# Performance work log

Measured on AMD Instinct MI355X. Metric: run time of the kernel, lower is better.

The kernel has to match this reference:

```python
import jax, jax.numpy as jnp
import numpy as np

B, T, C, H, D = 4, 2048, 1024, 16, 64
EPS = 1e-5

def setup_inputs() -> dict:
    key = jax.random.key(0)
    ks = jax.random.split(key, 8)
    s = lambda fan_in: 1.0 / np.sqrt(fan_in)
    return {
        'x': jax.random.normal(ks[0], (B, T, C), jnp.float32),
        'wq': jax.random.normal(ks[1], (H, C, D), jnp.float32) * s(C),
        'wk': jax.random.normal(ks[2], (H, C, D), jnp.float32) * s(C),
        'wv': jax.random.normal(ks[3], (H, C, D), jnp.float32) * s(C),
        'w_proj': jax.random.normal(ks[4], (C, C), jnp.float32) * s(C),
        'b_proj': jnp.zeros((C,), jnp.float32),
        'w1': jax.random.normal(ks[5], (C, 4 * C), jnp.float32) * s(C),
        'b1': jnp.zeros((4 * C,), jnp.float32),
        'w2': jax.random.normal(ks[6], (4 * C, C), jnp.float32) * s(4 * C),
        'b2': jnp.zeros((C,), jnp.float32),
        'g1': jnp.ones((C,), jnp.float32),
        'be1': jnp.zeros((C,), jnp.float32),
        'g2': jnp.ones((C,), jnp.float32),
        'be2': jnp.zeros((C,), jnp.float32),
    }

def layer_norm(x, g, b):
    mu = jnp.mean(x, axis=-1, keepdims=True)
    var = jnp.mean(jnp.square(x - mu), axis=-1, keepdims=True)
    return (x - mu) * jax.lax.rsqrt(var + EPS) * g + b

def reference(x, wq, wk, wv, w_proj, b_proj, w1, b1, w2, b2, g1, be1, g2, be2):
    # --- attention (pre-LN) ---
    xn = layer_norm(x, g1, be1)
    q = jnp.einsum('btc,hcd->bhtd', xn, wq)
    k = jnp.einsum('btc,hcd->bhtd', xn, wk)
    v = jnp.einsum('btc,hcd->bhtd', xn, wv)
    # NOTE: original scales by full embedding dim C (not head size)
    scores = jnp.einsum('bhtd,bhsd->bhts', q, k) * (C ** -0.5)
    causal = jnp.tril(jnp.ones((T, T), bool))
    scores = jnp.where(causal, scores, -jnp.inf)
    wei = jax.nn.softmax(scores, axis=-1)
    attn = jnp.einsum('bhts,bhsd->bhtd', wei, v)
    attn = attn.transpose(0, 2, 1, 3).reshape(B, T, C)  # concat heads
    x = x + attn @ w_proj + b_proj
    # --- FFN (pre-LN) ---
    xn2 = layer_norm(x, g2, be2)
    h = jax.nn.relu(xn2 @ w1 + b1)
    x = x + h @ w2 + b2
    return x
```

## Files before the change

kernel.cpp:

```cpp
#include <hip/hip_runtime.h>
#include <hip/hip_bf16.h>

#define B_ 4
#define T_ 2048
#define C_ 1024
#define H_ 16
#define D_ 64
#define M_ (B_*T_)

typedef unsigned short ushort;
typedef __attribute__((ext_vector_type(8))) short short8;
typedef __attribute__((ext_vector_type(8))) unsigned short ushort8;
typedef __attribute__((ext_vector_type(4))) float floatx4;
typedef __attribute__((ext_vector_type(4))) unsigned int uintx4;

static __device__ __forceinline__ float bf2f(ushort u) {
    unsigned int x = ((unsigned int)u) << 16;
    return __builtin_bit_cast(float, x);
}
static __device__ __forceinline__ ushort f2bf(float f) {
    unsigned int x = __builtin_bit_cast(unsigned int, f);
    unsigned int r = (x + 0x7fffu + ((x >> 16) & 1u)) >> 16;
    return (ushort)r;
}

typedef const __attribute__((address_space(1))) unsigned int gu32;
typedef __attribute__((address_space(3))) unsigned int lu32;
static __device__ __forceinline__ void glds16(const void* g, void* l) {
    __builtin_amdgcn_global_load_lds((gu32*)g, (lu32*)l, 16, 0, 0);
}

__global__ __launch_bounds__(256) void ln_kernel(
    const float* __restrict__ x, const float* __restrict__ g,
    const float* __restrict__ be, ushort* __restrict__ out)
{
    int row = blockIdx.x;
    int tid = threadIdx.x;
    const float* xr = x + (size_t)row * C_;
    float v[4];
    float s = 0.f, s2 = 0.f;
#pragma unroll
    for (int i = 0; i < 4; i++) {
        float t = xr[tid + i * 256];
        v[i] = t; s += t; s2 += t * t;
    }
#pragma unroll
    for (int off = 32; off; off >>= 1) {
        s  += __shfl_down(s, off);
        s2 += __shfl_down(s2, off);
    }
    __shared__ float rs[4], rs2[4];
    __shared__ float smu, srstd;
    int w = tid >> 6;
    if ((tid & 63) == 0) { rs[w] = s; rs2[w] = s2; }
    __syncthreads();
    if (tid == 0) {
        float ts  = rs[0] + rs[1] + rs[2] + rs[3];
        float ts2 = rs2[0] + rs2[1] + rs2[2] + rs2[3];
        float mu  = ts * (1.f / C_);
        float var = ts2 * (1.f / C_) - mu * mu;
        smu = mu; srstd = rsqrtf(var + 1e-5f);
    }
    __syncthreads();
    float mu = smu, r = srstd;
#pragma unroll
    for (int i = 0; i < 4; i++) {
        int c = tid + i * 256;
        out[(size_t)row * C_ + c] = f2bf((v[i] - mu) * r * g[c] + be[c]);
    }
}

static __device__ __forceinline__ void do_transpose(
    const float* __restrict__ in, ushort* __restrict__ out,
    int R, int Cn, int bx, int by)
{
    __shared__ float tile[32][33];
    int tx = threadIdx.x;
    int ty = threadIdx.y;
    int c0 = bx * 32, r0 = by * 32;
#pragma unroll
    for (int i = 0; i < 32; i += 8) {
        tile[ty + i][tx] = in[(size_t)(r0 + ty + i) * Cn + c0 + tx];
    }
    __syncthreads();
#pragma unroll
    for (int i = 0; i < 32; i += 8) {
        int oc = c0 + ty + i;
        int orr = r0 + tx;
        out[(size_t)oc * R + orr] = f2bf(tile[tx][ty + i]);
    }
}

__global__ __launch_bounds__(256) void wt_fused_kernel(
    const float* __restrict__ wq, const float* __restrict__ wk, const float* __restrict__ wv,
    const float* __restrict__ w_proj, const float* __restrict__ w1, const float* __restrict__ w2,
    ushort* __restrict__ WqkvT, ushort* __restrict__ WprojT,
    ushort* __restrict__ W1T, ushort* __restrict__ W2T)
{
    int id = blockIdx.x;
    if (id < 3072) {
        int which = id >> 10;
        int lid = id & 1023;
        int bz = lid >> 6;
        int rem = lid & 63;
        int by = rem >> 1, bx = rem & 1;
        const float* in = (which == 0 ? wq : which == 1 ? wk : wv) + (size_t)bz * C_ * D_;
        ushort* out = WqkvT + (size_t)which * C_ * C_ + (size_t)bz * D_ * C_;
        do_transpose(in, out, C_, D_, bx, by);
    } else if (id < 4096) {
        int lid = id - 3072;
        do_transpose(w_proj, WprojT, C_, C_, lid & 31, lid >> 5);
    } else if (id < 8192) {
        int lid = id - 4096;
        do_transpose(w1, W1T, C_, 4 * C_, lid & 127, lid >> 7);
    } else {
        int lid = id - 8192;
        do_transpose(w2, W2T, 4 * C_, C_, lid & 31, lid >> 5);
    }
}

__global__ __launch_bounds__(256) void vtrans_kernel(
    const ushort* __restrict__ qkv, ushort* __restrict__ VtG)
{
    int bh = blockIdx.y;
    int b = bh >> 4, h = bh & 15;
    int j0 = blockIdx.x * 64;
    int tid = threadIdx.x;
    __shared__ unsigned int X[64 * 33];
    const ushort* Vg = qkv + (size_t)(b * T_) * 3072 + 2048 + h * 64;
#pragma unroll
    for (int it = 0; it < 2; it++) {
        int j = (tid >> 3) + it * 32;
        int dp = (tid & 7) * 4;
        uintx4 val = *(const uintx4*)(Vg + (size_t)(j0 + j) * 3072 + dp * 2);
#pragma unroll
        for (int k = 0; k < 4; k++) X[j * 33 + dp + k] = val[k];
    }
    __syncthreads();
    int dp = tid >> 3, jc = tid & 7;
    unsigned int v[8];
#pragma unroll
    for (int jj = 0; jj < 8; jj++) v[jj] = X[(jc * 8 + jj) * 33 + dp];
    ushort8 lo, hi;
#pragma unroll
    for (int jj = 0; jj < 8; jj++) {
        lo[jj] = (ushort)(v[jj] & 0xffffu);
        hi[jj] = (ushort)(v[jj] >> 16);
    }
    size_t r0 = ((size_t)(h * 256 + 4 * (2 * dp) + b)) * T_ + j0 + jc * 8;
    size_t r1 = ((size_t)(h * 256 + 4 * (2 * dp + 1) + b)) * T_ + j0 + jc * 8;
    *(ushort8*)&VtG[r0] = lo;
    *(ushort8*)&VtG[r1] = hi;
}

template<bool OUTBF16, bool BIAS, bool RELU, bool RESID, bool DBUF>
__global__ __launch_bounds__(256, 2) void gemm_kernel(
    const ushort* __restrict__ A,
    const ushort* __restrict__ Bt,
    const float* __restrict__ bias,
    const float* __restrict__ resid,
    void* __restrict__ Cout,
    int Ndim, int K, int Nt)
{
    constexpr int NB = DBUF ? 2 : 1;
    __shared__ ushort As[NB][128 * 64];
    __shared__ ushort Bs[NB][128 * 64];
    int bid = blockIdx.x;
    int xcd = bid & 7;
    int loc = bid >> 3;
    int m0 = (xcd * 8 + (loc & 7)) * 128;
    int n0 = (loc >> 3) * 128;

    int tid = threadIdx.x;
    int wave = tid >> 6, lane = tid & 63;
    int quad = lane >> 4, l16 = lane & 15;
    int wm = (wave >> 1) * 64, wn = (wave & 1) * 64;
    floatx4 acc[4][4] = {};

    int lrow = lane >> 3;
    int lchunk = (lane & 7) ^ (lrow & 7);
    const ushort* Ab = A  + (size_t)m0 * K + lchunk * 8;
    const ushort* Bb = Bt + (size_t)n0 * K + lchunk * 8;

    int nK = K >> 6;
    if (DBUF) {
#pragma unroll
        for (int it = 0; it < 4; it++) {
            int rb = wave * 32 + it * 8;
            int r  = rb + lrow;
            glds16(Ab + (size_t)r * K, &As[0][rb * 64]);
            glds16(Bb + (size_t)r * K, &Bs[0][rb * 64]);
        }
    }

    for (int ki = 0; ki < nK; ki++) {
        int buf = DBUF ? (ki & 1) : 0;
        __syncthreads();
        if (DBUF) {
            if (ki + 1 < nK) {
                int kn = (ki + 1) * 64;
#pragma unroll
                for (int it = 0; it < 4; it++) {
                    int rb = wave * 32 + it * 8;
                    int r  = rb + lrow;
                    glds16(Ab + (size_t)r * K + kn, &As[buf ^ 1][rb * 64]);
                    glds16(Bb + (size_t)r * K + kn, &Bs[buf ^ 1][rb * 64]);
                }
            }
        } else {
            int kn = ki * 64;
#pragma unroll
            for (int it = 0; it < 4; it++) {
                int rb = wave * 32 + it * 8;
                int r  = rb + lrow;
                glds16(Ab + (size_t)r * K + kn, &As[0][rb * 64]);
                glds16(Bb + (size_t)r * K + kn, &Bs[0][rb * 64]);
            }
            __syncthreads();
        }
#pragma unroll
        for (int kk = 0; kk < 2; kk++) {
            short8 af[4], bfv[4];
            int c = kk * 4 + quad;
            int sw = (c ^ (l16 & 7)) * 8;
#pragma unroll
            for (int mi = 0; mi < 4; mi++)
                af[mi] = *(const short8*)&As[buf][(wm + mi * 16 + l16) * 64 + sw];
#pragma unroll
            for (int ni = 0; ni < 4; ni++)
                bfv[ni] = *(const short8*)&Bs[buf][(wn + ni * 16 + l16) * 64 + sw];
#pragma unroll
            for (int mi = 0; mi < 4; mi++)
#pragma unroll
                for (int ni = 0; ni < 4; ni++)
                    acc[mi][ni] = __builtin_amdgcn_mfma_f32_16x16x32_bf16(af[mi], bfv[ni], acc[mi][ni], 0, 0, 0);
        }
    }

    int r4 = quad * 4;
#pragma unroll
    for (int mi = 0; mi < 4; mi++) {
#pragma unroll
        for (int ni = 0; ni < 4; ni++) {
#pragma unroll
            for (int r = 0; r < 4; r++) {
                int gm = m0 + wm + mi * 16 + r4 + r;
                int gn = n0 + wn + ni * 16 + l16;
                float v = acc[mi][ni][r];
                if (BIAS)  v += bias[gn];
                if (RESID) v += resid[(size_t)gm * Ndim + gn];
                if (RELU)  v = fmaxf(v, 0.f);
                if (OUTBF16) ((ushort*)Cout)[(size_t)gm * Ndim + gn] = f2bf(v);
                else         ((float*)Cout)[(size_t)gm * Ndim + gn] = v;
            }
        }
    }
}

__global__ __launch_bounds__(256, 2) void attn_kernel(
    const ushort* __restrict__ qkv,
    const ushort* __restrict__ VtG,
    ushort* __restrict__ attnb)
{
    const int LD = 3072;
    int bid = blockIdx.x;
    int bh = (bid & 7) * 8 + ((bid >> 3) & 7);
    int qt = 15 - (bid >> 6);
    int b = bh >> 4, h = bh & 15;
    int t0 = qt * 128;
    int tid = threadIdx.x;
    int wave = tid >> 6, lane = tid & 63;
    int quad = lane >> 4, l16 = lane & 15;

    __shared__ ushort Ks[2][64 * 64];
    __shared__ ushort Vt[2][64 * 64];
    __shared__ ushort Ps[4][32 * 72];

    const ushort* Qg = qkv + (size_t)(b * T_) * LD + h * 64;
    const ushort* Kg = Qg + 1024;
    const ushort* VtB = VtG + (size_t)(h * 256 + b) * T_;

    int qrow_base = t0 + wave * 32;
    int lrow = lane >> 3;
    int lchunk = (lane & 7) ^ (lrow & 7);

    short8 qa[2][2];
#pragma unroll
    for (int mt = 0; mt < 2; mt++) {
        const ushort* qp = Qg + (size_t)(qrow_base + mt * 16 + l16) * LD + quad * 8;
        ushort8 q0 = *(const ushort8*)qp;
        ushort8 q1 = *(const ushort8*)(qp + 32);
        ushort8 a0, a1;
#pragma unroll
        for (int d = 0; d < 8; d++) {
            a0[d] = f2bf(bf2f(q0[d]) * 0.03125f);
            a1[d] = f2bf(bf2f(q1[d]) * 0.03125f);
        }
        qa[mt][0] = __builtin_bit_cast(short8, a0);
        qa[mt][1] = __builtin_bit_cast(short8, a1);
    }

    float l_part[2][4];
    floatx4 o_acc[2][4];
#pragma unroll
    for (int mt = 0; mt < 2; mt++)
#pragma unroll
        for (int r = 0; r < 4; r++) {
            l_part[mt][r] = 0.f;
            o_acc[mt][r] = floatx4{0.f, 0.f, 0.f, 0.f};
        }

    int nIter = t0 / 64 + 2;

#pragma unroll
    for (int it = 0; it < 2; it++) {
        int rb = (wave * 2 + it) * 8;
        int r = rb + lrow;
        glds16(Kg  + (size_t)r * LD + lchunk * 8, &Ks[0][rb * 64]);
        glds16(VtB + (size_t)r * (4 * T_) + lchunk * 8, &Vt[0][rb * 64]);
    }

    for (int ii = 0; ii < nIter; ii++) {
        int s0 = ii * 64;
        int buf = ii & 1;
        __syncthreads();
        if (ii + 1 < nIter) {
            int sn = s0 + 64;
#pragma unroll
            for (int it = 0; it < 2; it++) {
                int rb = (wave * 2 + it) * 8;
                int r = rb + lrow;
                glds16(Kg  + (size_t)(sn + r) * LD + lchunk * 8, &Ks[buf ^ 1][rb * 64]);
                glds16(VtB + (size_t)r * (4 * T_) + sn + lchunk * 8, &Vt[buf ^ 1][rb * 64]);
            }
        }

        if (s0 <= qrow_base + 31) {
#pragma unroll
            for (int mt = 0; mt < 2; mt++) {
                floatx4 s_acc[4];
#pragma unroll
                for (int nt = 0; nt < 4; nt++) {
                    int krow = nt * 16 + l16;
                    const short8* kb0 = (const short8*)&Ks[buf][krow * 64 + ((quad       ^ (l16 & 7)) * 8)];
                    const short8* kb1 = (const short8*)&Ks[buf][krow * 64 + (((4 + quad) ^ (l16 & 7)) * 8)];
                    floatx4 z = {0.f, 0.f, 0.f, 0.f};
                    z = __builtin_amdgcn_mfma_f32_16x16x32_bf16(qa[mt][0], *kb0, z, 0, 0, 0);
                    s_acc[nt] = __builtin_amdgcn_mfma_f32_16x16x32_bf16(qa[mt][1], *kb1, z, 0, 0, 0);
                }
                int base_mt = qrow_base + mt * 16;
                if (s0 + 63 > base_mt) {
#pragma unroll
                    for (int nt = 0; nt < 4; nt++)
#pragma unroll
                        for (int r = 0; r < 4; r++) {
                            int gi = base_mt + quad * 4 + r;
                            int gj = s0 + nt * 16 + l16;
                            if (gj > gi) s_acc[nt][r] = -INFINITY;
                        }
                }
#pragma unroll
                for (int nt = 0; nt < 4; nt++)
#pragma unroll
                    for (int r = 0; r < 4; r++) {
                        float e = __expf(s_acc[nt][r]);
                        s_acc[nt][r] = e;
                        l_part[mt][r] += e;
                        Ps[wave][(mt * 16 + quad * 4 + r) * 72 + nt * 16 + l16] = f2bf(e);
                    }
            }
            asm volatile("s_waitcnt lgkmcnt(0)" ::: "memory");
            short8 pa[2][2];
#pragma unroll
            for (int mt = 0; mt < 2; mt++) {
                pa[mt][0] = *(const short8*)&Ps[wave][(mt * 16 + l16) * 72 + quad * 8];
                pa[mt][1] = *(const short8*)&Ps[wave][(mt * 16 + l16) * 72 + quad * 8 + 32];
            }
#pragma unroll
            for (int dt = 0; dt < 4; dt++) {
                int vrow = dt * 16 + l16;
                const short8* vb0 = (const short8*)&Vt[buf][vrow * 64 + ((quad       ^ (l16 & 7)) * 8)];
                const short8* vb1 = (const short8*)&Vt[buf][vrow * 64 + (((4 + quad) ^ (l16 & 7)) * 8)];
#pragma unroll
                for (int mt = 0; mt < 2; mt++) {
                    o_acc[mt][dt] = __builtin_amdgcn_mfma_f32_16x16x32_bf16(pa[mt][0], *vb0, o_acc[mt][dt], 0, 0, 0);
                    o_acc[mt][dt] = __builtin_amdgcn_mfma_f32_16x16x32_bf16(pa[mt][1], *vb1, o_acc[mt][dt], 0, 0, 0);
                }
            }
        }
    }

#pragma unroll
    for (int mt = 0; mt < 2; mt++)
#pragma unroll
        for (int r = 0; r < 4; r++) {
            float ls = l_part[mt][r];
            ls += __shfl_xor(ls, 1);
            ls += __shfl_xor(ls, 2);
            ls += __shfl_xor(ls, 4);
            ls += __shfl_xor(ls, 8);
            float inv = 1.f / ls;
            int gi = qrow_base + mt * 16 + quad * 4 + r;
            ushort* op = attnb + (size_t)(b * T_ + gi) * 1024 + h * 64;
#pragma unroll
            for (int dt = 0; dt < 4; dt++)
                op[dt * 16 + l16] = f2bf(o_acc[mt][dt][r] * inv);
        }
}

extern "C" void kernel_launch(void* const* d_in, const int* in_sizes, int n_in,
                              void* d_out, int out_size, void* d_ws, size_t ws_size,
                              hipStream_t stream) {
    (void)in_sizes; (void)n_in; (void)out_size; (void)ws_size;
    const float* x      = (const float*)d_in[0];
    const float* wq     = (const float*)d_in[1];
    const float* wk     = (const float*)d_in[2];
    const float* wv     = (const float*)d_in[3];
    const float* w_proj = (const float*)d_in[4];
    const float* b_proj = (const float*)d_in[5];
    const float* w1     = (const float*)d_in[6];
    const float* b1     = (const float*)d_in[7];
    const float* w2     = (const float*)d_in[8];
    const float* b2     = (const float*)d_in[9];
    const float* g1     = (const float*)d_in[10];
    const float* be1    = (const float*)d_in[11];
    const float* g2     = (const float*)d_in[12];
    const float* be2    = (const float*)d_in[13];
    float* out = (float*)d_out;

    char* ws = (char*)d_ws;
    const size_t MB = 1024ull * 1024ull;
    ushort* xn     = (ushort*)(ws + 0);
    ushort* qkv    = (ushort*)(ws + 16 * MB);
    ushort* attnb  = (ushort*)(ws + 64 * MB);
    ushort* hbuf   = (ushort*)(ws + 16 * MB);
    float*  x1     = (float*) (ws + 80 * MB);
    ushort* VtG    = (ushort*)(ws + 80 * MB);
    ushort* WqkvT  = (ushort*)(ws + 112 * MB);
    ushort* WprojT = (ushort*)(ws + 118 * MB);
    ushort* W1T    = (ushort*)(ws + 120 * MB);
    ushort* W2T    = (ushort*)(ws + 128 * MB);
    ushort* xn2 = xn;

    ln_kernel<<<M_, 256, 0, stream>>>(x, g1, be1, xn);
    wt_fused_kernel<<<12288, dim3(32, 8), 0, stream>>>(
        wq, wk, wv, w_proj, w1, w2, WqkvT, WprojT, W1T, W2T);
    gemm_kernel<true, false, false, false, false><<<64 * 24, 256, 0, stream>>>(
        xn, WqkvT, nullptr, nullptr, qkv, 3072, C_, 24);
    vtrans_kernel<<<dim3(T_ / 64, B_ * H_), 256, 0, stream>>>(qkv, VtG);
    attn_kernel<<<1024, 256, 0, stream>>>(qkv, VtG, attnb);
    gemm_kernel<false, true, false, true, true><<<64 * 8, 256, 0, stream>>>(
        attnb, WprojT, b_proj, x, x1, C_, C_, 8);
    ln_kernel<<<M_, 256, 0, stream>>>(x1, g2, be2, xn2);
    gemm_kernel<true, true, true, false, false><<<64 * 32, 256, 0, stream>>>(
        xn2, W1T, b1, nullptr, hbuf, 4 * C_, C_, 32);
    gemm_kernel<false, true, false, true, true><<<64 * 8, 256, 0, stream>>>(
        hbuf, W2T, b2, x1, out, C_, 4 * C_, 8);
}
```

Baseline: 465.8 us.

## Fuse LN1 into weight prep kernel and double attention query tile to 256 rows

The first LayerNorm and the weight transpose/convert are merged into one launch, with blocks dispatched by ID range, which removes a kernel launch. The attention kernel now processes 256 query rows per block (64 per wave) instead of 128, so each K/V tile loaded into LDS is reused across twice as many queries. The grid is halved to 512 blocks and launch bounds ask for 3 blocks per CU. The risks are higher register pressure from the doubled accumulators and coarser causal load balance with fewer, larger blocks.

```diff
diff --git a/kernel.cpp b/kernel.cpp
--- a/kernel.cpp
+++ b/kernel.cpp
@@ -30,12 +30,10 @@
     __builtin_amdgcn_global_load_lds((gu32*)g, (lu32*)l, 16, 0, 0);
 }
 
-__global__ __launch_bounds__(256) void ln_kernel(
+static __device__ __forceinline__ void ln_body(
     const float* __restrict__ x, const float* __restrict__ g,
-    const float* __restrict__ be, ushort* __restrict__ out)
-{
-    int row = blockIdx.x;
-    int tid = threadIdx.x;
+    const float* __restrict__ be, ushort* __restrict__ out, int row, int tid)
+{
     const float* xr = x + (size_t)row * C_;
     float v[4];
     float s = 0.f, s2 = 0.f;
@@ -70,13 +68,20 @@
     }
 }
 
+__global__ __launch_bounds__(256) void ln_kernel(
+    const float* __restrict__ x, const float* __restrict__ g,
+    const float* __restrict__ be, ushort* __restrict__ out)
+{
+    ln_body(x, g, be, out, blockIdx.x, threadIdx.x);
+}
+
 static __device__ __forceinline__ void do_transpose(
     const float* __restrict__ in, ushort* __restrict__ out,
-    int R, int Cn, int bx, int by)
+    int R, int Cn, int bx, int by, int tid)
 {
     __shared__ float tile[32][33];
-    int tx = threadIdx.x;
-    int ty = threadIdx.y;
+    int tx = tid & 31;
+    int ty = tid >> 5;
     int c0 = bx * 32, r0 = by * 32;
 #pragma unroll
     for (int i = 0; i < 32; i += 8) {
@@ -91,31 +96,37 @@
     }
 }
 
-__global__ __launch_bounds__(256) void wt_fused_kernel(
+__global__ __launch_bounds__(256) void prep_fused_kernel(
+    const float* __restrict__ x, const float* __restrict__ g1, const float* __restrict__ be1,
+    ushort* __restrict__ xn,
     const float* __restrict__ wq, const float* __restrict__ wk, const float* __restrict__ wv,
     const float* __restrict__ w_proj, const float* __restrict__ w1, const float* __restrict__ w2,
     ushort* __restrict__ WqkvT, ushort* __restrict__ WprojT,
     ushort* __restrict__ W1T, ushort* __restrict__ W2T)
 {
     int id = blockIdx.x;
-    if (id < 3072) {
-        int which = id >> 10;
-        int lid = id & 1023;
-        int bz = lid >> 6;
-        int rem = lid & 63;
+    int tid = threadIdx.x;
+    if (id < 8192) {
+        ln_body(x, g1, be1, xn, id, tid);
+    } else if (id < 11264) {
+        int lid = id - 8192;
+        int which = lid >> 10;
+        int l2 = lid & 1023;
+        int bz = l2 >> 6;
+        int rem = l2 & 63;
         int by = rem >> 1, bx = rem & 1;
         const float* in = (which == 0 ? wq : which == 1 ? wk : wv) + (size_t)bz * C_ * D_;
         ushort* out = WqkvT + (size_t)which * C_ * C_ + (size_t)bz * D_ * C_;
-        do_transpose(in, out, C_, D_, bx, by);
-    } else if (id < 4096) {
-        int lid = id - 3072;
-        do_transpose(w_proj, WprojT, C_, C_, lid & 31, lid >> 5);
-    } else if (id < 8192) {
-        int lid = id - 4096;
-        do_transpose(w1, W1T, C_, 4 * C_, lid & 127, lid >> 7);
+        do_transpose(in, out, C_, D_, bx, by, tid);
+    } else if (id < 12288) {
+        int lid = id - 11264;
+        do_transpose(w_proj, WprojT, C_, C_, lid & 31, lid >> 5, tid);
+    } else if (id < 16384) {
+        int lid = id - 12288;
+        do_transpose(w1, W1T, C_, 4 * C_, lid & 127, lid >> 7, tid);
     } else {
-        int lid = id - 8192;
-        do_transpose(w2, W2T, 4 * C_, C_, lid & 31, lid >> 5);
+        int lid = id - 16384;
+        do_transpose(w2, W2T, 4 * C_, C_, lid & 31, lid >> 5, tid);
     }
 }
 
@@ -257,7 +268,7 @@
     }
 }
 
-__global__ __launch_bounds__(256, 2) void attn_kernel(
+__global__ __launch_bounds__(256, 3) void attn_kernel(
     const ushort* __restrict__ qkv,
     const ushort* __restrict__ VtG,
     ushort* __restrict__ attnb)
@@ -265,9 +276,9 @@
     const int LD = 3072;
     int bid = blockIdx.x;
     int bh = (bid & 7) * 8 + ((bid >> 3) & 7);
-    int qt = 15 - (bid >> 6);
+    int qt = 7 - (bid >> 6);
     int b = bh >> 4, h = bh & 15;
-    int t0 = qt * 128;
+    int t0 = qt * 256;
     int tid = threadIdx.x;
     int wave = tid >> 6, lane = tid & 63;
     int quad = lane >> 4, l16 = lane & 15;
@@ -280,13 +291,13 @@
     const ushort* Kg = Qg + 1024;
     const ushort* VtB = VtG + (size_t)(h * 256 + b) * T_;
 
-    int qrow_base = t0 + wave * 32;
+    int qrow_base = t0 + wave * 64;
     int lrow = lane >> 3;
     int lchunk = (lane & 7) ^ (lrow & 7);
 
-    short8 qa[2][2];
-#pragma unroll
-    for (int mt = 0; mt < 2; mt++) {
+    short8 qa[4][2];
+#pragma unroll
+    for (int mt = 0; mt < 4; mt++) {
         const ushort* qp = Qg + (size_t)(qrow_base + mt * 16 + l16) * LD + quad * 8;
         ushort8 q0 = *(const ushort8*)qp;
         ushort8 q1 = *(const ushort8*)(qp + 32);
@@ -300,17 +311,17 @@
         qa[mt][1] = __builtin_bit_cast(short8, a1);
     }
 
-    float l_part[2][4];
-    floatx4 o_acc[2][4];
-#pragma unroll
-    for (int mt = 0; mt < 2; mt++)
+    float l_part[4][4];
+    floatx4 o_acc[4][4];
+#pragma unroll
+    for (int mt = 0; mt < 4; mt++)
 #pragma unroll
         for (int r = 0; r < 4; r++) {
             l_part[mt][r] = 0.f;
             o_acc[mt][r] = floatx4{0.f, 0.f, 0.f, 0.f};
         }
 
-    int nIter = t0 / 64 + 2;
+    int nIter = t0 / 64 + 4;
 
 #pragma unroll
     for (int it = 0; it < 2; it++) {
@@ -335,63 +346,67 @@
             }
         }
 
-        if (s0 <= qrow_base + 31) {
-#pragma unroll
-            for (int mt = 0; mt < 2; mt++) {
-                floatx4 s_acc[4];
-#pragma unroll
-                for (int nt = 0; nt < 4; nt++) {
-                    int krow = nt * 16 + l16;
-                    const short8* kb0 = (const short8*)&Ks[buf][krow * 64 + ((quad       ^ (l16 & 7)) * 8)];
-                    const short8* kb1 = (const short8*)&Ks[buf][krow * 64 + (((4 + quad) ^ (l16 & 7)) * 8)];
-                    floatx4 z = {0.f, 0.f, 0.f, 0.f};
-                    z = __builtin_amdgcn_mfma_f32_16x16x32_bf16(qa[mt][0], *kb0, z, 0, 0, 0);
-                    s_acc[nt] = __builtin_amdgcn_mfma_f32_16x16x32_bf16(qa[mt][1], *kb1, z, 0, 0, 0);
-                }
-                int base_mt = qrow_base + mt * 16;
-                if (s0 + 63 > base_mt) {
+        if (s0 <= qrow_base + 63) {
+#pragma unroll
+            for (int h2 = 0; h2 < 2; h2++) {
+#pragma unroll
+                for (int mt2 = 0; mt2 < 2; mt2++) {
+                    int mt = h2 * 2 + mt2;
+                    floatx4 s_acc[4];
+#pragma unroll
+                    for (int nt = 0; nt < 4; nt++) {
+                        int krow = nt * 16 + l16;
+                        const short8* kb0 = (const short8*)&Ks[buf][krow * 64 + ((quad       ^ (l16 & 7)) * 8)];
+                        const short8* kb1 = (const short8*)&Ks[buf][krow * 64 + (((4 + quad) ^ (l16 & 7)) * 8)];
+                        floatx4 z = {0.f, 0.f, 0.f, 0.f};
+                        z = __builtin_amdgcn_mfma_f32_16x16x32_bf16(qa[mt][0], *kb0, z, 0, 0, 0);
+                        s_acc[nt] = __builtin_amdgcn_mfma_f32_16x16x32_bf16(qa[mt][1], *kb1, z, 0, 0, 0);
+                    }
+                    int base_mt = qrow_base + mt * 16;
+                    if (s0 + 63 > base_mt) {
+#pragma unroll
+                        for (int nt = 0; nt < 4; nt++)
+#pragma unroll
+                            for (int r = 0; r < 4; r++) {
+                                int gi = base_mt + quad * 4 + r;
+                                int gj = s0 + nt * 16 + l16;
+                                if (gj > gi) s_acc[nt][r] = -INFINITY;
+                            }
+                    }
 #pragma unroll
                     for (int nt = 0; nt < 4; nt++)
 #pragma unroll
                         for (int r = 0; r < 4; r++) {
-                            int gi = base_mt + quad * 4 + r;
-                            int gj = s0 + nt * 16 + l16;
-                            if (gj > gi) s_acc[nt][r] = -INFINITY;
+                            float e = __expf(s_acc[nt][r]);
+                            l_part[mt][r] += e;
+                            Ps[wave][(mt2 * 16 + quad * 4 + r) * 72 + nt * 16 + l16] = f2bf(e);
                         }
                 }
-#pragma unroll
-                for (int nt = 0; nt < 4; nt++)
-#pragma unroll
-                    for (int r = 0; r < 4; r++) {
-                        float e = __expf(s_acc[nt][r]);
-                        s_acc[nt][r] = e;
-                        l_part[mt][r] += e;
-                        Ps[wave][(mt * 16 + quad * 4 + r) * 72 + nt * 16 + l16] = f2bf(e);
+                asm volatile("s_waitcnt lgkmcnt(0)" ::: "memory");
+                short8 pa[2][2];
+#pragma unroll
+                for (int mt2 = 0; mt2 < 2; mt2++) {
+                    pa[mt2][0] = *(const short8*)&Ps[wave][(mt2 * 16 + l16) * 72 + quad * 8];
+                    pa[mt2][1] = *(const short8*)&Ps[wave][(mt2 * 16 + l16) * 72 + quad * 8 + 32];
+                }
+#pragma unroll
+                for (int dt = 0; dt < 4; dt++) {
+                    int vrow = dt * 16 + l16;
+                    const short8* vb0 = (const short8*)&Vt[buf][vrow * 64 + ((quad       ^ (l16 & 7)) * 8)];
+                    const short8* vb1 = (const short8*)&Vt[buf][vrow * 64 + (((4 + quad) ^ (l16 & 7)) * 8)];
+#pragma unroll
+                    for (int mt2 = 0; mt2 < 2; mt2++) {
+                        int mt = h2 * 2 + mt2;
+                        o_acc[mt][dt] = __builtin_amdgcn_mfma_f32_16x16x32_bf16(pa[mt2][0], *vb0, o_acc[mt][dt], 0, 0, 0);
+                        o_acc[mt][dt] = __builtin_amdgcn_mfma_f32_16x16x32_bf16(pa[mt2][1], *vb1, o_acc[mt][dt], 0, 0, 0);
                     }
-            }
-            asm volatile("s_waitcnt lgkmcnt(0)" ::: "memory");
-            short8 pa[2][2];
-#pragma unroll
-            for (int mt = 0; mt < 2; mt++) {
-                pa[mt][0] = *(const short8*)&Ps[wave][(mt * 16 + l16) * 72 + quad * 8];
-                pa[mt][1] = *(const short8*)&Ps[wave][(mt * 16 + l16) * 72 + quad * 8 + 32];
-            }
-#pragma unroll
-            for (int dt = 0; dt < 4; dt++) {
-                int vrow = dt * 16 + l16;
-                const short8* vb0 = (const short8*)&Vt[buf][vrow * 64 + ((quad       ^ (l16 & 7)) * 8)];
-                const short8* vb1 = (const short8*)&Vt[buf][vrow * 64 + (((4 + quad) ^ (l16 & 7)) * 8)];
-#pragma unroll
-                for (int mt = 0; mt < 2; mt++) {
-                    o_acc[mt][dt] = __builtin_amdgcn_mfma_f32_16x16x32_bf16(pa[mt][0], *vb0, o_acc[mt][dt], 0, 0, 0);
-                    o_acc[mt][dt] = __builtin_amdgcn_mfma_f32_16x16x32_bf16(pa[mt][1], *vb1, o_acc[mt][dt], 0, 0, 0);
                 }
             }
         }
     }
 
 #pragma unroll
-    for (int mt = 0; mt < 2; mt++)
+    for (int mt = 0; mt < 4; mt++)
 #pragma unroll
         for (int r = 0; r < 4; r++) {
             float ls = l_part[mt][r];
@@ -442,13 +457,12 @@
     ushort* W2T    = (ushort*)(ws + 128 * MB);
     ushort* xn2 = xn;
 
-    ln_kernel<<<M_, 256, 0, stream>>>(x, g1, be1, xn);
-    wt_fused_kernel<<<12288, dim3(32, 8), 0, stream>>>(
-        wq, wk, wv, w_proj, w1, w2, WqkvT, WprojT, W1T, W2T);
+    prep_fused_kernel<<<20480, 256, 0, stream>>>(
+        x, g1, be1, xn, wq, wk, wv, w_proj, w1, w2, WqkvT, WprojT, W1T, W2T);
     gemm_kernel<true, false, false, false, false><<<64 * 24, 256, 0, stream>>>(
         xn, WqkvT, nullptr, nullptr, qkv, 3072, C_, 24);
     vtrans_kernel<<<dim3(T_ / 64, B_ * H_), 256, 0, stream>>>(qkv, VtG);
-    attn_kernel<<<1024, 256, 0, stream>>>(qkv, VtG, attnb);
+    attn_kernel<<<512, 256, 0, stream>>>(qkv, VtG, attnb);
     gemm_kernel<false, true, false, true, true><<<64 * 8, 256, 0, stream>>>(
         attnb, WprojT, b_proj, x, x1, C_, C_, 8);
     ln_kernel<<<M_, 256, 0, stream>>>(x1, g2, be2, xn2);
```

Measured after the change: 568.3 us. +22.0%, slower.
